# Optimization experiments

Hardware: AMD Instinct MI355X
Metric: run time of the kernel (lower is better)

The kernel has to match this reference:

```python
import jax, jax.numpy as jnp
import numpy as np

N_NODES = 100000
N_EDGES = 1000000
IN_DIM = 64
OUT_DIM = 64
EDGE_DIM = 16
LN_EPS = 1e-5
GINE_EPS = 0.0  # PyG GINEConv default eps


def setup_inputs() -> dict:
    key = jax.random.key(0)
    ks = jax.random.split(key, 10)
    s = lambda d: 1.0 / np.sqrt(d)
    x = jax.random.normal(ks[0], (N_NODES, IN_DIM), dtype=jnp.float32)
    edge_index = jax.random.randint(ks[1], (2, N_EDGES), 0, N_NODES, dtype=jnp.int64)
    edge_attr = jax.random.normal(ks[2], (N_EDGES, EDGE_DIM), dtype=jnp.float32)
    # GINEConv internal edge projection Linear(edge_dim, in_dim)
    We = jax.random.uniform(ks[3], (EDGE_DIM, IN_DIM), jnp.float32, -s(EDGE_DIM), s(EDGE_DIM))
    be = jax.random.uniform(ks[4], (IN_DIM,), jnp.float32, -s(EDGE_DIM), s(EDGE_DIM))
    # MLP: Linear(in_dim, out_dim) -> ReLU -> Linear(out_dim, out_dim)
    W1 = jax.random.uniform(ks[5], (IN_DIM, OUT_DIM), jnp.float32, -s(IN_DIM), s(IN_DIM))
    b1 = jax.random.uniform(ks[6], (OUT_DIM,), jnp.float32, -s(IN_DIM), s(IN_DIM))
    W2 = jax.random.uniform(ks[7], (OUT_DIM, OUT_DIM), jnp.float32, -s(OUT_DIM), s(OUT_DIM))
    b2 = jax.random.uniform(ks[8], (OUT_DIM,), jnp.float32, -s(OUT_DIM), s(OUT_DIM))
    ln_gamma = jnp.ones((OUT_DIM,), jnp.float32)
    ln_beta = jnp.zeros((OUT_DIM,), jnp.float32)
    return {"x": x, "edge_index": edge_index, "edge_attr": edge_attr,
            "We": We, "be": be, "W1": W1, "b1": b1, "W2": W2, "b2": b2,
            "ln_gamma": ln_gamma, "ln_beta": ln_beta}


def reference(x, edge_index, edge_attr, We, be, W1, b1, W2, b2, ln_gamma, ln_beta):
    src, dst = edge_index[0], edge_index[1]
    # message: ReLU(x_j + lin(edge_attr))  [E, IN_DIM]
    msg = jax.nn.relu(x[src] + edge_attr @ We + be)
    # scatter-sum into target nodes  [N, IN_DIM]
    aggr = jax.ops.segment_sum(msg, dst, num_segments=x.shape[0])
    h = (1.0 + GINE_EPS) * x + aggr
    # MLP
    h = jax.nn.relu(h @ W1 + b1) @ W2 + b2
    # LayerNorm over last dim
    mu = jnp.mean(h, axis=-1, keepdims=True)
    var = jnp.var(h, axis=-1, keepdims=True)
    h = (h - mu) * jax.lax.rsqrt(var + LN_EPS) * ln_gamma + ln_beta
    return jax.nn.relu(h)
```

## Files before the change

kernel.cpp:

```cpp
#include <hip/hip_runtime.h>

typedef short short8 __attribute__((ext_vector_type(8)));
typedef float f32x4 __attribute__((ext_vector_type(4)));

__device__ __forceinline__ float bf2f(unsigned short b) {
    union { unsigned u; float f; } c;
    c.u = ((unsigned)b) << 16;
    return c.f;
}

__device__ __forceinline__ unsigned short f2bf(float x) {
    union { float f; unsigned u; } c;
    c.f = x;
    unsigned u = c.u;
    u += 0x7fffu + ((u >> 16) & 1u);
    return (unsigned short)(u >> 16);
}

__device__ __forceinline__ float loadf(const void* p, long long i, unsigned isbf) {
    if (isbf) return bf2f(((const unsigned short*)p)[i]);
    return ((const float*)p)[i];
}

__device__ __forceinline__ f32x4 mfma16(short8 a, short8 b, f32x4 c) {
    return __builtin_amdgcn_mfma_f32_16x16x32_bf16(a, b, c, 0, 0, 0);
}

__device__ __forceinline__ float dotbf(uint4 ea, uint4 eb, const float* Wcol) {
    unsigned wds[8] = {ea.x, ea.y, ea.z, ea.w, eb.x, eb.y, eb.z, eb.w};
    float acc = 0.f;
    #pragma unroll
    for (int q = 0; q < 8; ++q) {
        union { unsigned u; float f; } clo, chi;
        clo.u = wds[q] << 16;
        chi.u = wds[q] & 0xffff0000u;
        acc += clo.f * Wcol[2 * q] + chi.f * Wcol[2 * q + 1];
    }
    return acc;
}

__device__ __forceinline__ float dotf32(const float* eap, const float* Wcol) {
    f32x4 e0 = ((const f32x4*)eap)[0];
    f32x4 e1 = ((const f32x4*)eap)[1];
    f32x4 e2 = ((const f32x4*)eap)[2];
    f32x4 e3 = ((const f32x4*)eap)[3];
    float ea[16] = {e0[0], e0[1], e0[2], e0[3],
                    e1[0], e1[1], e1[2], e1[3],
                    e2[0], e2[1], e2[2], e2[3],
                    e3[0], e3[1], e3[2], e3[3]};
    float acc = 0.f;
    #pragma unroll
    for (int k = 0; k < 16; ++k) acc += ea[k] * Wcol[k];
    return acc;
}

__global__ void gine_flag_kernel(const unsigned* gm_bits, const unsigned* ei_bits,
                                 unsigned* flags) {
    if (blockIdx.x == 0 && threadIdx.x == 0) {
        flags[0] = (gm_bits[0] == 0x3F803F80u) ? 1u : 0u;
        unsigned o = 0;
        for (int k = 0; k < 8; ++k) o |= ei_bits[2 * k + 1];
        flags[1] = (o == 0u) ? 1u : 0u;
    }
}

__global__ void gine_zero_kernel(float* p, int n) {
    int t = blockIdx.x * blockDim.x + threadIdx.x;
    if (t < n) p[t] = 0.0f;
}

__global__ void gine_prep_kernel(const void* W1, const void* b1,
                                 const void* W2, const void* b2,
                                 const void* gm, const void* bt,
                                 const void* We, const void* be,
                                 const unsigned* flags,
                                 unsigned short* W1B, unsigned short* W2B,
                                 float* vecs) {
    int t = blockIdx.x * blockDim.x + threadIdx.x;
    unsigned isbf = flags[0];
    if (t < 8192) {
        int which = t >> 12;
        int u = t & 4095;
        int j = u & 7, L = (u >> 3) & 63, ktnt = u >> 9;
        int kt = ktnt >> 2, nt = ktnt & 3;
        int k = kt * 32 + (L >> 4) * 8 + j;
        int c = nt * 16 + (L & 15);
        const void* W = which ? W2 : W1;
        unsigned short v = f2bf(loadf(W, k * 64 + c, isbf));
        if (which) W2B[u] = v; else W1B[u] = v;
    } else if (t < 8448) {
        int u = t - 8192;
        const void* s = (u < 64) ? b1 : (u < 128) ? b2 : (u < 192) ? gm : bt;
        vecs[u] = loadf(s, u & 63, isbf);
    } else if (t < 8512) {
        vecs[256 + (t - 8448)] = loadf(be, t - 8448, isbf);
    } else if (t < 9536) {
        int u = t - 8512;
        vecs[320 + u] = loadf(We, u, isbf);
    }
}

__global__ void gine_hist_kernel(const void* edge_index, const unsigned* flags,
                                 int* count, int E, int N) {
    int t = blockIdx.x * blockDim.x + threadIdx.x;
    int stride = gridDim.x * blockDim.x;
    unsigned is64 = flags[1];
    for (int e = t; e < E; e += stride) {
        long long dst = is64 ? ((const long long*)edge_index)[E + e]
                             : (long long)((const int*)edge_index)[E + e];
        if (dst >= 0 && dst < N) atomicAdd(&count[(int)dst], 1);
    }
}

__global__ void gine_scan1_kernel(const int* count, int* row_start, int* bsum,
                                  int N) {
    __shared__ int s[256];
    int t = threadIdx.x;
    int i = blockIdx.x * 256 + t;
    int v = (i < N) ? count[i] : 0;
    s[t] = v;
    __syncthreads();
    for (int off = 1; off < 256; off <<= 1) {
        int u = (t >= off) ? s[t - off] : 0;
        __syncthreads();
        s[t] += u;
        __syncthreads();
    }
    if (i < N) row_start[i] = s[t] - v;
    if (t == 255) bsum[blockIdx.x] = s[255];
}

__global__ void gine_scan2_kernel(int* bsum, int* bscan, int* row_start,
                                  int nb, int N) {
    __shared__ int s[512];
    int t = threadIdx.x;
    int v = (t < nb) ? bsum[t] : 0;
    s[t] = v;
    __syncthreads();
    for (int off = 1; off < 512; off <<= 1) {
        int u = (t >= off) ? s[t - off] : 0;
        __syncthreads();
        s[t] += u;
        __syncthreads();
    }
    if (t < nb) bscan[t] = s[t] - v;
    if (t == nb - 1) row_start[N] = s[t];
}

__global__ void gine_scan3_kernel(int* row_start, int* cursor,
                                  const int* bscan, int N) {
    int i = blockIdx.x * 256 + threadIdx.x;
    if (i < N) {
        int r = row_start[i] + bscan[blockIdx.x];
        row_start[i] = r;
        cursor[i] = r;
    }
}

__global__ void gine_scatter_kernel(const void* edge_index, const unsigned* flags,
                                    int* cursor, unsigned long long* sorted,
                                    int E, int N) {
    int t = blockIdx.x * blockDim.x + threadIdx.x;
    int stride = gridDim.x * blockDim.x;
    unsigned is64 = flags[1];
    for (int e = t; e < E; e += stride) {
        long long src, dst;
        if (is64) {
            src = ((const long long*)edge_index)[e];
            dst = ((const long long*)edge_index)[E + e];
        } else {
            src = ((const int*)edge_index)[e];
            dst = ((const int*)edge_index)[E + e];
        }
        if (dst < 0 || dst >= N) continue;
        if (src < 0) src = 0;
        if (src >= N) src = N - 1;
        int pos = atomicAdd(&cursor[(int)dst], 1);
        sorted[pos] = ((unsigned long long)(unsigned)e << 32) | (unsigned long long)(unsigned)src;
    }
}

__global__ __launch_bounds__(256, 4) void gine_gather_kernel(
        const void* x, const void* edge_attr,
        const unsigned long long* sorted,
        const int* row_start, const float* vecs,
        const unsigned* flags, float* h, int N) {
    int w = threadIdx.x >> 6;
    int lane = threadIdx.x & 63;
    int gw = blockIdx.x * 4 + w;
    int nwaves = gridDim.x * 4;
    unsigned isbf = flags[0];

    float Wcol[16];
    #pragma unroll
    for (int k = 0; k < 16; ++k) Wcol[k] = vecs[320 + k * 64 + lane];
    float bev = vecs[256 + lane];

    if (isbf) {
        const unsigned short* xb  = (const unsigned short*)x;
        const unsigned short* eab = (const unsigned short*)edge_attr;
        for (int v = gw; v < N; v += nwaves) {
            int beg = row_start[v];
            int end = row_start[v + 1];
            float a0 = bf2f(xb[(size_t)v * 64 + lane]);
            float a1 = 0.f, a2 = 0.f, a3 = 0.f;
            int i = beg;
            for (; i + 4 <= end; i += 4) {
                unsigned long long c0 = sorted[i];
                unsigned long long c1 = sorted[i + 1];
                unsigned long long c2 = sorted[i + 2];
                unsigned long long c3 = sorted[i + 3];
                int src0 = (int)(c0 & 0xffffffffULL), eid0 = (int)(c0 >> 32);
                int src1 = (int)(c1 & 0xffffffffULL), eid1 = (int)(c1 >> 32);
                int src2 = (int)(c2 & 0xffffffffULL), eid2 = (int)(c2 >> 32);
                int src3 = (int)(c3 & 0xffffffffULL), eid3 = (int)(c3 >> 32);

                float xv0 = bf2f(xb[(size_t)src0 * 64 + lane]);
                float xv1 = bf2f(xb[(size_t)src1 * 64 + lane]);
                float xv2 = bf2f(xb[(size_t)src2 * 64 + lane]);
                float xv3 = bf2f(xb[(size_t)src3 * 64 + lane]);

                const uint4* p0 = (const uint4*)(eab + (size_t)eid0 * 16);
                const uint4* p1 = (const uint4*)(eab + (size_t)eid1 * 16);
                const uint4* p2 = (const uint4*)(eab + (size_t)eid2 * 16);
                const uint4* p3 = (const uint4*)(eab + (size_t)eid3 * 16);
                uint4 e00 = p0[0], e01 = p0[1];
                uint4 e10 = p1[0], e11 = p1[1];
                uint4 e20 = p2[0], e21 = p2[1];
                uint4 e30 = p3[0], e31 = p3[1];

                float m0 = dotbf(e00, e01, Wcol);
                float m1 = dotbf(e10, e11, Wcol);
                float m2 = dotbf(e20, e21, Wcol);
                float m3 = dotbf(e30, e31, Wcol);
                m0 += bev + xv0; if (m0 < 0.f) m0 = 0.f; a0 += m0;
                m1 += bev + xv1; if (m1 < 0.f) m1 = 0.f; a1 += m1;
                m2 += bev + xv2; if (m2 < 0.f) m2 = 0.f; a2 += m2;
                m3 += bev + xv3; if (m3 < 0.f) m3 = 0.f; a3 += m3;
            }
            for (; i < end; ++i) {
                unsigned long long c = sorted[i];
                int src = (int)(c & 0xffffffffULL);
                int eid = (int)(c >> 32);
                float xv = bf2f(xb[(size_t)src * 64 + lane]);
                const uint4* p0 = (const uint4*)(eab + (size_t)eid * 16);
                uint4 e0 = p0[0], e1 = p0[1];
                float m = dotbf(e0, e1, Wcol);
                m += bev + xv;
                if (m < 0.f) m = 0.f;
                a0 += m;
            }
            h[(long long)v * 64 + lane] = (a0 + a1) + (a2 + a3);
        }
    } else {
        const float* xf  = (const float*)x;
        const float* eaf = (const float*)edge_attr;
        for (int v = gw; v < N; v += nwaves) {
            int beg = row_start[v];
            int end = row_start[v + 1];
            float a0 = xf[(size_t)v * 64 + lane];
            float a1 = 0.f;
            int i = beg;
            for (; i + 2 <= end; i += 2) {
                unsigned long long c0 = sorted[i];
                unsigned long long c1 = sorted[i + 1];
                int src0 = (int)(c0 & 0xffffffffULL), eid0 = (int)(c0 >> 32);
                int src1 = (int)(c1 & 0xffffffffULL), eid1 = (int)(c1 >> 32);
                float xv0 = xf[(size_t)src0 * 64 + lane];
                float xv1 = xf[(size_t)src1 * 64 + lane];
                float m0 = dotf32(eaf + (size_t)eid0 * 16, Wcol);
                float m1 = dotf32(eaf + (size_t)eid1 * 16, Wcol);
                m0 += bev + xv0; if (m0 < 0.f) m0 = 0.f; a0 += m0;
                m1 += bev + xv1; if (m1 < 0.f) m1 = 0.f; a1 += m1;
            }
            for (; i < end; ++i) {
                unsigned long long c = sorted[i];
                int src = (int)(c & 0xffffffffULL);
                int eid = (int)(c >> 32);
                float xv = xf[(size_t)src * 64 + lane];
                float m = dotf32(eaf + (size_t)eid * 16, Wcol);
                m += bev + xv;
                if (m < 0.f) m = 0.f;
                a0 += m;
            }
            h[(long long)v * 64 + lane] = a0 + a1;
        }
    }
}

__global__ void GINEBlock_49795850830259_kernel(
    const void* x, const void* edge_index, const void* edge_attr,
    const void* We, const void* be, const unsigned* flags,
    float* aggr, int E, int N, int n0, int n1) {
    int wid  = (blockIdx.x * blockDim.x + threadIdx.x) >> 6;
    int lane = threadIdx.x & 63;
    if (wid >= E) return;

    unsigned isbf = flags[0];
    unsigned is64 = flags[1];

    long long src, dst;
    if (is64) {
        src = ((const long long*)edge_index)[wid];
        dst = ((const long long*)edge_index)[E + wid];
    } else {
        src = ((const int*)edge_index)[wid];
        dst = ((const int*)edge_index)[E + wid];
    }
    if (src < 0 || src >= N || dst < n0 || dst >= n1) return;

    float eav = 0.0f;
    if (lane < 16) eav = loadf(edge_attr, (long long)wid * 16 + lane, isbf);

    float acc = loadf(be, lane, isbf);
    for (int k = 0; k < 16; ++k)
        acc += __shfl(eav, k, 64) * loadf(We, k * 64 + lane, isbf);

    acc += loadf(x, src * 64 + lane, isbf);
    if (acc < 0.0f) acc = 0.0f;

    atomicAdd(aggr + (dst - n0) * 64 + lane, acc);
}

__global__ void gine_addx_kernel(const void* x, float* aggr,
                                 const unsigned* flags, int n0, int n1) {
    int t = blockIdx.x * blockDim.x + threadIdx.x;
    int total = (n1 - n0) * 64;
    if (t >= total) return;
    unsigned isbf = flags[0];
    aggr[t] += loadf(x, (long long)n0 * 64 + t, isbf);
}

__global__ __launch_bounds__(256) void gine_node_mfma_kernel(
    const float* h, const unsigned short* W1B, const unsigned short* W2B,
    const float* vecs, const unsigned* flags, void* out, int n0, int n1) {
    __shared__ float Tlds[4][16 * 68];
    int w = threadIdx.x >> 6;
    int L = threadIdx.x & 63;
    int g = L >> 4, m = L & 15;
    int nb = n0 + (blockIdx.x * 4 + w) * 16;
    if (nb >= n1) return;
    unsigned isbf = flags[0];

    const float* b1f = vecs;
    const float* b2f = vecs + 64;
    const float* gmf = vecs + 128;
    const float* btf = vecs + 192;

    int node = nb + m;
    if (node >= n1) node = n1 - 1;
    long long rel = node - n0;

    short8 ahi[2], alo[2];
    for (int kt = 0; kt < 2; ++kt) {
        int fb = kt * 32 + g * 8;
        const float* hp = h + rel * 64 + fb;
        f32x4 a0 = *(const f32x4*)hp;
        f32x4 a1 = *(const f32x4*)(hp + 4);
        for (int j = 0; j < 8; ++j) {
            float hv = (j < 4) ? a0[j] : a1[j - 4];
            unsigned short hb = f2bf(hv);
            float lo = hv - bf2f(hb);
            ahi[kt][j] = (short)hb;
            alo[kt][j] = (short)f2bf(lo);
        }
    }

    float t16[16];
    for (int nt = 0; nt < 4; ++nt) {
        short8 bp0 = *(const short8*)(W1B + ((size_t)(0 * 4 + nt) * 64 + L) * 8);
        short8 bp1 = *(const short8*)(W1B + ((size_t)(1 * 4 + nt) * 64 + L) * 8);
        f32x4 acc = {0.f, 0.f, 0.f, 0.f};
        acc = mfma16(ahi[0], bp0, acc);
        acc = mfma16(ahi[1], bp1, acc);
        acc = mfma16(alo[0], bp0, acc);
        acc = mfma16(alo[1], bp1, acc);
        float bias = b1f[nt * 16 + m];
        for (int r = 0; r < 4; ++r) {
            float v = acc[r] + bias;
            t16[nt * 4 + r] = v > 0.f ? v : 0.f;
        }
    }

    float* tl = Tlds[w];
    for (int nt = 0; nt < 4; ++nt)
        for (int r = 0; r < 4; ++r)
            tl[(g * 4 + r) * 68 + nt * 16 + m] = t16[nt * 4 + r];

    short8 thi[2], tlo[2];
    for (int kt = 0; kt < 2; ++kt) {
        const float* rp = tl + m * 68 + kt * 32 + g * 8;
        f32x4 v0 = *(const f32x4*)rp;
        f32x4 v1 = *(const f32x4*)(rp + 4);
        for (int j = 0; j < 8; ++j) {
            float hv = (j < 4) ? v0[j] : v1[j - 4];
            unsigned short hb = f2bf(hv);
            float lo = hv - bf2f(hb);
            thi[kt][j] = (short)hb;
            tlo[kt][j] = (short)f2bf(lo);
        }
    }

    float o16[16];
    for (int nt = 0; nt < 4; ++nt) {
        short8 bp0 = *(const short8*)(W2B + ((size_t)(0 * 4 + nt) * 64 + L) * 8);
        short8 bp1 = *(const short8*)(W2B + ((size_t)(1 * 4 + nt) * 64 + L) * 8);
        f32x4 acc = {0.f, 0.f, 0.f, 0.f};
        acc = mfma16(thi[0], bp0, acc);
        acc = mfma16(thi[1], bp1, acc);
        acc = mfma16(tlo[0], bp0, acc);
        acc = mfma16(tlo[1], bp1, acc);
        float bias = b2f[nt * 16 + m];
        for (int r = 0; r < 4; ++r) o16[nt * 4 + r] = acc[r] + bias;
    }

    for (int r = 0; r < 4; ++r) {
        float s = o16[r] + o16[4 + r] + o16[8 + r] + o16[12 + r];
        s += __shfl_xor(s, 1, 64);
        s += __shfl_xor(s, 2, 64);
        s += __shfl_xor(s, 4, 64);
        s += __shfl_xor(s, 8, 64);
        float mu = s * (1.0f / 64.0f);
        float v = 0.f;
        for (int nt = 0; nt < 4; ++nt) {
            float d = o16[nt * 4 + r] - mu;
            v += d * d;
        }
        v += __shfl_xor(v, 1, 64);
        v += __shfl_xor(v, 2, 64);
        v += __shfl_xor(v, 4, 64);
        v += __shfl_xor(v, 8, 64);
        float inv = rsqrtf(v * (1.0f / 64.0f) + 1e-5f);
        int nodeR = nb + g * 4 + r;
        if (nodeR < n1) {
            for (int nt = 0; nt < 4; ++nt) {
                int c = nt * 16 + m;
                float rr = (o16[nt * 4 + r] - mu) * inv * gmf[c] + btf[c];
                if (rr < 0.f) rr = 0.f;
                long long oidx = (long long)nodeR * 64 + c;
                if (isbf) ((unsigned short*)out)[oidx] = f2bf(rr);
                else      ((float*)out)[oidx] = rr;
            }
        }
    }
}

static inline size_t align256(size_t a) { return (a + 255) & ~(size_t)255; }

extern "C" void kernel_launch(void* const* d_in, const int* in_sizes, int n_in,
                              void* d_out, int out_size, void* d_ws, size_t ws_size,
                              hipStream_t stream) {
    const void* x          = d_in[0];
    const void* edge_index = d_in[1];
    const void* edge_attr  = d_in[2];
    const void* We         = d_in[3];
    const void* be         = d_in[4];
    const void* W1         = d_in[5];
    const void* b1         = d_in[6];
    const void* W2         = d_in[7];
    const void* b2         = d_in[8];
    const void* gm         = d_in[9];
    const void* bt         = d_in[10];

    const int N = in_sizes[0] / 64;
    const int E = in_sizes[1] / 2;

    unsigned* flags     = (unsigned*)d_ws;
    unsigned short* W1B = (unsigned short*)((char*)d_ws + 256);
    unsigned short* W2B = W1B + 4096;
    float* vecs         = (float*)(W2B + 4096);
    int* bsum           = (int*)((char*)d_ws + 24576);
    int* bscan          = bsum + 1024;

    gine_flag_kernel<<<1, 64, 0, stream>>>((const unsigned*)gm,
                                           (const unsigned*)edge_index, flags);
    gine_prep_kernel<<<38, 256, 0, stream>>>(W1, b1, W2, b2, gm, bt, We, be,
                                             flags, W1B, W2B, vecs);

    int nb = (N + 255) / 256;
    int node_blocks = (N + 63) / 64;
    int gblocks = (N + 15) / 16;
    if (gblocks > 6250) gblocks = 6250;

    size_t o_count  = 32768;
    size_t o_row    = o_count + align256((size_t)N * 4);
    size_t o_cursor = o_row + align256((size_t)(N + 1) * 4);
    size_t o_sorted = o_cursor + align256((size_t)N * 4);
    size_t o_h      = o_sorted + align256((size_t)E * 8);
    size_t need     = o_h + (size_t)N * 256;

    if (ws_size >= need && nb <= 512) {
        int* count    = (int*)((char*)d_ws + o_count);
        int* row_start= (int*)((char*)d_ws + o_row);
        int* cursor   = (int*)((char*)d_ws + o_cursor);
        unsigned long long* sorted = (unsigned long long*)((char*)d_ws + o_sorted);
        float* h      = (float*)((char*)d_ws + o_h);

        gine_zero_kernel<<<(N + 255) / 256, 256, 0, stream>>>((float*)count, N);
        gine_hist_kernel<<<1024, 256, 0, stream>>>(edge_index, flags, count, E, N);
        gine_scan1_kernel<<<nb, 256, 0, stream>>>(count, row_start, bsum, N);
        gine_scan2_kernel<<<1, 512, 0, stream>>>(bsum, bscan, row_start, nb, N);
        gine_scan3_kernel<<<nb, 256, 0, stream>>>(row_start, cursor, bscan, N);
        gine_scatter_kernel<<<1024, 256, 0, stream>>>(edge_index, flags, cursor,
                                                      sorted, E, N);
        gine_gather_kernel<<<gblocks, 256, 0, stream>>>(x, edge_attr, sorted,
                                                        row_start, vecs, flags, h, N);
        gine_node_mfma_kernel<<<node_blocks, 256, 0, stream>>>(
            h, W1B, W2B, vecs, flags, d_out, 0, N);
        return;
    }

    float* aggr = (float*)((char*)d_ws + 32768);
    long long usable = (ws_size > 32768) ? (long long)(ws_size - 32768) : 0;
    long long ncll = (usable / 256) & ~63LL;
    int NC = (ncll > N) ? N : (int)ncll;
    if (NC < 64) return;

    long long edge_threads = (long long)E * 64;
    int edge_blocks = (int)((edge_threads + 255) / 256);

    for (int n0 = 0; n0 < N; n0 += NC) {
        int n1 = n0 + NC; if (n1 > N) n1 = N;
        int chunk = n1 - n0;
        int n_aggr = chunk * 64;

        gine_zero_kernel<<<(n_aggr + 255) / 256, 256, 0, stream>>>(aggr, n_aggr);
        GINEBlock_49795850830259_kernel<<<edge_blocks, 256, 0, stream>>>(
            x, edge_index, edge_attr, We, be, flags, aggr, E, N, n0, n1);
        gine_addx_kernel<<<(n_aggr + 255) / 256, 256, 0, stream>>>(
            x, aggr, flags, n0, n1);
        int chunk_blocks = (chunk + 63) / 64;
        gine_node_mfma_kernel<<<chunk_blocks, 256, 0, stream>>>(
            aggr, W1B, W2B, vecs, flags, d_out, n0, n1);
    }
}
```

Measured before the change: 465.9 us.

## Permute edge attributes into destination-sorted order during scatter for contiguous gather reads

The scatter kernel now also copies each edge's bf16 attribute row into a buffer indexed by its sorted position, so the gather kernel reads edge attributes contiguously instead of through random edge ids. This converts the random edge_attr reads in the gather into streaming reads, at the cost of an extra 32 MB write and read plus a random-destination write during the scatter. The gather unroll drops from 4 to 2 and the occupancy hint is removed. The new path runs only when the workspace is large enough and the input is bf16.

Result: no change. 460.6 us, median of 2 (-1.1%).

```diff
diff --git a/kernel.cpp b/kernel.cpp
--- a/kernel.cpp
+++ b/kernel.cpp
@@ -180,9 +180,43 @@
     }
 }
 
-__global__ __launch_bounds__(256, 4) void gine_gather_kernel(
+__global__ void gine_scatter2_kernel(const void* edge_index, const void* edge_attr,
+                                     const unsigned* flags,
+                                     int* cursor, unsigned long long* sorted,
+                                     unsigned short* ea_perm, int E, int N) {
+    int t = blockIdx.x * blockDim.x + threadIdx.x;
+    int stride = gridDim.x * blockDim.x;
+    unsigned is64 = flags[1];
+    unsigned isbf = flags[0];
+    for (int e = t; e < E; e += stride) {
+        long long src, dst;
+        if (is64) {
+            src = ((const long long*)edge_index)[e];
+            dst = ((const long long*)edge_index)[E + e];
+        } else {
+            src = ((const int*)edge_index)[e];
+            dst = ((const int*)edge_index)[E + e];
+        }
+        if (dst < 0 || dst >= N) continue;
+        if (src < 0) src = 0;
+        if (src >= N) src = N - 1;
+        int pos = atomicAdd(&cursor[(int)dst], 1);
+        sorted[pos] = ((unsigned long long)(unsigned)e << 32) | (unsigned long long)(unsigned)src;
+        if (isbf) {
+            const uint4* er = (const uint4*)((const unsigned short*)edge_attr
+                                             + (size_t)e * 16);
+            uint4 r0 = er[0];
+            uint4 r1 = er[1];
+            uint4* wp = (uint4*)(ea_perm + (size_t)pos * 16);
+            wp[0] = r0;
+            wp[1] = r1;
+        }
+    }
+}
+
+__global__ __launch_bounds__(256) void gine_gather2_kernel(
         const void* x, const void* edge_attr,
-        const unsigned long long* sorted,
+        const unsigned long long* sorted, const unsigned short* ea_perm,
         const int* row_start, const float* vecs,
         const unsigned* flags, float* h, int N) {
     int w = threadIdx.x >> 6;
@@ -197,60 +231,43 @@
     float bev = vecs[256 + lane];
 
     if (isbf) {
-        const unsigned short* xb  = (const unsigned short*)x;
-        const unsigned short* eab = (const unsigned short*)edge_attr;
+        const unsigned short* xb = (const unsigned short*)x;
         for (int v = gw; v < N; v += nwaves) {
             int beg = row_start[v];
             int end = row_start[v + 1];
             float a0 = bf2f(xb[(size_t)v * 64 + lane]);
-            float a1 = 0.f, a2 = 0.f, a3 = 0.f;
+            float a1 = 0.f;
             int i = beg;
-            for (; i + 4 <= end; i += 4) {
+            for (; i + 2 <= end; i += 2) {
                 unsigned long long c0 = sorted[i];
                 unsigned long long c1 = sorted[i + 1];
-                unsigned long long c2 = sorted[i + 2];
-                unsigned long long c3 = sorted[i + 3];
-                int src0 = (int)(c0 & 0xffffffffULL), eid0 = (int)(c0 >> 32);
-                int src1 = (int)(c1 & 0xffffffffULL), eid1 = (int)(c1 >> 32);
-                int src2 = (int)(c2 & 0xffffffffULL), eid2 = (int)(c2 >> 32);
-                int src3 = (int)(c3 & 0xffffffffULL), eid3 = (int)(c3 >> 32);
+                int src0 = (int)(c0 & 0xffffffffULL);
+                int src1 = (int)(c1 & 0xffffffffULL);
+
+                const uint4* p = (const uint4*)(ea_perm + (size_t)i * 16);
+                uint4 e00 = p[0], e01 = p[1];
+                uint4 e10 = p[2], e11 = p[3];
 
                 float xv0 = bf2f(xb[(size_t)src0 * 64 + lane]);
                 float xv1 = bf2f(xb[(size_t)src1 * 64 + lane]);
-                float xv2 = bf2f(xb[(size_t)src2 * 64 + lane]);
-                float xv3 = bf2f(xb[(size_t)src3 * 64 + lane]);
-
-                const uint4* p0 = (const uint4*)(eab + (size_t)eid0 * 16);
-                const uint4* p1 = (const uint4*)(eab + (size_t)eid1 * 16);
-                const uint4* p2 = (const uint4*)(eab + (size_t)eid2 * 16);
-                const uint4* p3 = (const uint4*)(eab + (size_t)eid3 * 16);
-                uint4 e00 = p0[0], e01 = p0[1];
-                uint4 e10 = p1[0], e11 = p1[1];
-                uint4 e20 = p2[0], e21 = p2[1];
-                uint4 e30 = p3[0], e31 = p3[1];
 
                 float m0 = dotbf(e00, e01, Wcol);
                 float m1 = dotbf(e10, e11, Wcol);
-                float m2 = dotbf(e20, e21, Wcol);
-                float m3 = dotbf(e30, e31, Wcol);
                 m0 += bev + xv0; if (m0 < 0.f) m0 = 0.f; a0 += m0;
                 m1 += bev + xv1; if (m1 < 0.f) m1 = 0.f; a1 += m1;
-                m2 += bev + xv2; if (m2 < 0.f) m2 = 0.f; a2 += m2;
-                m3 += bev + xv3; if (m3 < 0.f) m3 = 0.f; a3 += m3;
             }
             for (; i < end; ++i) {
                 unsigned long long c = sorted[i];
                 int src = (int)(c & 0xffffffffULL);
-                int eid = (int)(c >> 32);
+                const uint4* p = (const uint4*)(ea_perm + (size_t)i * 16);
+                uint4 e0 = p[0], e1 = p[1];
                 float xv = bf2f(xb[(size_t)src * 64 + lane]);
-                const uint4* p0 = (const uint4*)(eab + (size_t)eid * 16);
-                uint4 e0 = p0[0], e1 = p0[1];
                 float m = dotbf(e0, e1, Wcol);
                 m += bev + xv;
                 if (m < 0.f) m = 0.f;
                 a0 += m;
             }
-            h[(long long)v * 64 + lane] = (a0 + a1) + (a2 + a3);
+            h[(long long)v * 64 + lane] = a0 + a1;
         }
     } else {
         const float* xf  = (const float*)x;
@@ -288,6 +305,114 @@
     }
 }
 
+__global__ __launch_bounds__(256, 4) void gine_gather_kernel(
+        const void* x, const void* edge_attr,
+        const unsigned long long* sorted,
+        const int* row_start, const float* vecs,
+        const unsigned* flags, float* h, int N) {
+    int w = threadIdx.x >> 6;
+    int lane = threadIdx.x & 63;
+    int gw = blockIdx.x * 4 + w;
+    int nwaves = gridDim.x * 4;
+    unsigned isbf = flags[0];
+
+    float Wcol[16];
+    #pragma unroll
+    for (int k = 0; k < 16; ++k) Wcol[k] = vecs[320 + k * 64 + lane];
+    float bev = vecs[256 + lane];
+
+    if (isbf) {
+        const unsigned short* xb  = (const unsigned short*)x;
+        const unsigned short* eab = (const unsigned short*)edge_attr;
+        for (int v = gw; v < N; v += nwaves) {
+            int beg = row_start[v];
+            int end = row_start[v + 1];
+            float a0 = bf2f(xb[(size_t)v * 64 + lane]);
+            float a1 = 0.f, a2 = 0.f, a3 = 0.f;
+            int i = beg;
+            for (; i + 4 <= end; i += 4) {
+                unsigned long long c0 = sorted[i];
+                unsigned long long c1 = sorted[i + 1];
+                unsigned long long c2 = sorted[i + 2];
+                unsigned long long c3 = sorted[i + 3];
+                int src0 = (int)(c0 & 0xffffffffULL), eid0 = (int)(c0 >> 32);
+                int src1 = (int)(c1 & 0xffffffffULL), eid1 = (int)(c1 >> 32);
+                int src2 = (int)(c2 & 0xffffffffULL), eid2 = (int)(c2 >> 32);
+                int src3 = (int)(c3 & 0xffffffffULL), eid3 = (int)(c3 >> 32);
+
+                float xv0 = bf2f(xb[(size_t)src0 * 64 + lane]);
+                float xv1 = bf2f(xb[(size_t)src1 * 64 + lane]);
+                float xv2 = bf2f(xb[(size_t)src2 * 64 + lane]);
+                float xv3 = bf2f(xb[(size_t)src3 * 64 + lane]);
+
+                const uint4* p0 = (const uint4*)(eab + (size_t)eid0 * 16);
+                const uint4* p1 = (const uint4*)(eab + (size_t)eid1 * 16);
+                const uint4* p2 = (const uint4*)(eab + (size_t)eid2 * 16);
+                const uint4* p3 = (const uint4*)(eab + (size_t)eid3 * 16);
+                uint4 e00 = p0[0], e01 = p0[1];
+                uint4 e10 = p1[0], e11 = p1[1];
+                uint4 e20 = p2[0], e21 = p2[1];
+                uint4 e30 = p3[0], e31 = p3[1];
+
+                float m0 = dotbf(e00, e01, Wcol);
+                float m1 = dotbf(e10, e11, Wcol);
+                float m2 = dotbf(e20, e21, Wcol);
+                float m3 = dotbf(e30, e31, Wcol);
+                m0 += bev + xv0; if (m0 < 0.f) m0 = 0.f; a0 += m0;
+                m1 += bev + xv1; if (m1 < 0.f) m1 = 0.f; a1 += m1;
+                m2 += bev + xv2; if (m2 < 0.f) m2 = 0.f; a2 += m2;
+                m3 += bev + xv3; if (m3 < 0.f) m3 = 0.f; a3 += m3;
+            }
+            for (; i < end; ++i) {
+                unsigned long long c = sorted[i];
+                int src = (int)(c & 0xffffffffULL);
+                int eid = (int)(c >> 32);
+                float xv = bf2f(xb[(size_t)src * 64 + lane]);
+                const uint4* p0 = (const uint4*)(eab + (size_t)eid * 16);
+                uint4 e0 = p0[0], e1 = p0[1];
+                float m = dotbf(e0, e1, Wcol);
+                m += bev + xv;
+                if (m < 0.f) m = 0.f;
+                a0 += m;
+            }
+            h[(long long)v * 64 + lane] = (a0 + a1) + (a2 + a3);
+        }
+    } else {
+        const float* xf  = (const float*)x;
+        const float* eaf = (const float*)edge_attr;
+        for (int v = gw; v < N; v += nwaves) {
+            int beg = row_start[v];
+            int end = row_start[v + 1];
+            float a0 = xf[(size_t)v * 64 + lane];
+            float a1 = 0.f;
+            int i = beg;
+            for (; i + 2 <= end; i += 2) {
+                unsigned long long c0 = sorted[i];
+                unsigned long long c1 = sorted[i + 1];
+                int src0 = (int)(c0 & 0xffffffffULL), eid0 = (int)(c0 >> 32);
+                int src1 = (int)(c1 & 0xffffffffULL), eid1 = (int)(c1 >> 32);
+                float xv0 = xf[(size_t)src0 * 64 + lane];
+                float xv1 = xf[(size_t)src1 * 64 + lane];
+                float m0 = dotf32(eaf + (size_t)eid0 * 16, Wcol);
+                float m1 = dotf32(eaf + (size_t)eid1 * 16, Wcol);
+                m0 += bev + xv0; if (m0 < 0.f) m0 = 0.f; a0 += m0;
+                m1 += bev + xv1; if (m1 < 0.f) m1 = 0.f; a1 += m1;
+            }
+            for (; i < end; ++i) {
+                unsigned long long c = sorted[i];
+                int src = (int)(c & 0xffffffffULL);
+                int eid = (int)(c >> 32);
+                float xv = xf[(size_t)src * 64 + lane];
+                float m = dotf32(eaf + (size_t)eid * 16, Wcol);
+                m += bev + xv;
+                if (m < 0.f) m = 0.f;
+                a0 += m;
+            }
+            h[(long long)v * 64 + lane] = a0 + a1;
+        }
+    }
+}
+
 __global__ void GINEBlock_49795850830259_kernel(
     const void* x, const void* edge_index, const void* edge_attr,
     const void* We, const void* be, const unsigned* flags,
@@ -486,25 +611,40 @@
     size_t o_row    = o_count + align256((size_t)N * 4);
     size_t o_cursor = o_row + align256((size_t)(N + 1) * 4);
     size_t o_sorted = o_cursor + align256((size_t)N * 4);
-    size_t o_h      = o_sorted + align256((size_t)E * 8);
-    size_t need     = o_h + (size_t)N * 256;
-
-    if (ws_size >= need && nb <= 512) {
+    size_t o_eap    = o_sorted + align256((size_t)E * 8);
+    size_t o_h1     = o_eap;
+    size_t o_h2     = o_eap + align256((size_t)E * 32);
+    size_t need1    = o_h1 + (size_t)N * 256;
+    size_t need2    = o_h2 + (size_t)N * 256;
+
+    if (ws_size >= need1 && nb <= 512) {
         int* count    = (int*)((char*)d_ws + o_count);
         int* row_start= (int*)((char*)d_ws + o_row);
         int* cursor   = (int*)((char*)d_ws + o_cursor);
         unsigned long long* sorted = (unsigned long long*)((char*)d_ws + o_sorted);
-        float* h      = (float*)((char*)d_ws + o_h);
+        bool tier2 = (ws_size >= need2);
+        unsigned short* ea_perm = (unsigned short*)((char*)d_ws + o_eap);
+        float* h = (float*)((char*)d_ws + (tier2 ? o_h2 : o_h1));
 
         gine_zero_kernel<<<(N + 255) / 256, 256, 0, stream>>>((float*)count, N);
         gine_hist_kernel<<<1024, 256, 0, stream>>>(edge_index, flags, count, E, N);
         gine_scan1_kernel<<<nb, 256, 0, stream>>>(count, row_start, bsum, N);
         gine_scan2_kernel<<<1, 512, 0, stream>>>(bsum, bscan, row_start, nb, N);
         gine_scan3_kernel<<<nb, 256, 0, stream>>>(row_start, cursor, bscan, N);
-        gine_scatter_kernel<<<1024, 256, 0, stream>>>(edge_index, flags, cursor,
-                                                      sorted, E, N);
-        gine_gather_kernel<<<gblocks, 256, 0, stream>>>(x, edge_attr, sorted,
-                                                        row_start, vecs, flags, h, N);
+        if (tier2) {
+            gine_scatter2_kernel<<<1024, 256, 0, stream>>>(edge_index, edge_attr,
+                                                           flags, cursor, sorted,
+                                                           ea_perm, E, N);
+            gine_gather2_kernel<<<gblocks, 256, 0, stream>>>(x, edge_attr, sorted,
+                                                             ea_perm, row_start,
+                                                             vecs, flags, h, N);
+        } else {
+            gine_scatter_kernel<<<1024, 256, 0, stream>>>(edge_index, flags, cursor,
+                                                          sorted, E, N);
+            gine_gather_kernel<<<gblocks, 256, 0, stream>>>(x, edge_attr, sorted,
+                                                            row_start, vecs, flags,
+                                                            h, N);
+        }
         gine_node_mfma_kernel<<<node_blocks, 256, 0, stream>>>(
             h, W1B, W2B, vecs, flags, d_out, 0, N);
         return;
```

## Sort edges by source and scatter messages via atomics instead of dst-gather

Applied to the files above, without the earlier changes.

Replaces the destination-sorted gather with a source-sorted 'spray': edges are bucketed by source node, each wave loads the source node's x row once and atomically adds ReLU messages into h rows of destination nodes, with h pre-initialised from x. The scatter step also copies edge_attr rows into source-sorted order, bf16 only, so the spray reads them contiguously. This trades per-edge random x reads for per-edge random fp32 atomic adds and an extra edge_attr copy, and the atomics make the summation order nondeterministic. The old path is kept as a fallback when the workspace is too small.

New measurement: 530.9 us, median of 2. 14.0% more time.

```diff
diff --git a/kernel.cpp b/kernel.cpp
--- a/kernel.cpp
+++ b/kernel.cpp
@@ -100,15 +100,49 @@
     }
 }
 
-__global__ void gine_hist_kernel(const void* edge_index, const unsigned* flags,
-                                 int* count, int E, int N) {
+__global__ void gine_hinit_kernel(const void* x, float* h,
+                                  const unsigned* flags, int total) {
+    int t = blockIdx.x * blockDim.x + threadIdx.x;
+    unsigned isbf = flags[0];
+    if (isbf) {
+        int i = t * 8;
+        if (i >= total) return;
+        uint4 v = *(const uint4*)((const unsigned short*)x + i);
+        unsigned wds[4] = {v.x, v.y, v.z, v.w};
+        #pragma unroll
+        for (int q = 0; q < 4; ++q) {
+            union { unsigned u; float f; } clo, chi;
+            clo.u = wds[q] << 16;
+            chi.u = wds[q] & 0xffff0000u;
+            h[i + 2 * q]     = clo.f;
+            h[i + 2 * q + 1] = chi.f;
+        }
+    } else {
+        int i = t * 4;
+        if (i >= total) return;
+        f32x4 v = *(const f32x4*)((const float*)x + i);
+        *(f32x4*)(h + i) = v;
+    }
+}
+
+__global__ void gine_histS_kernel(const void* edge_index, const unsigned* flags,
+                                  int* count, int E, int N) {
     int t = blockIdx.x * blockDim.x + threadIdx.x;
     int stride = gridDim.x * blockDim.x;
     unsigned is64 = flags[1];
     for (int e = t; e < E; e += stride) {
-        long long dst = is64 ? ((const long long*)edge_index)[E + e]
-                             : (long long)((const int*)edge_index)[E + e];
-        if (dst >= 0 && dst < N) atomicAdd(&count[(int)dst], 1);
+        long long src, dst;
+        if (is64) {
+            src = ((const long long*)edge_index)[e];
+            dst = ((const long long*)edge_index)[E + e];
+        } else {
+            src = ((const int*)edge_index)[e];
+            dst = ((const int*)edge_index)[E + e];
+        }
+        if (dst < 0 || dst >= N) continue;
+        if (src < 0) src = 0;
+        if (src >= N) src = N - 1;
+        atomicAdd(&count[(int)src], 1);
     }
 }
 
@@ -154,6 +188,122 @@
         int r = row_start[i] + bscan[blockIdx.x];
         row_start[i] = r;
         cursor[i] = r;
+    }
+}
+
+__global__ void gine_scatterS_kernel(const void* edge_index, const void* edge_attr,
+                                     const unsigned* flags, int* cursor,
+                                     unsigned long long* meta,
+                                     unsigned short* eaS, int E, int N) {
+    int t = blockIdx.x * blockDim.x + threadIdx.x;
+    int stride = gridDim.x * blockDim.x;
+    unsigned is64 = flags[1];
+    unsigned isbf = flags[0];
+    for (int e = t; e < E; e += stride) {
+        long long src, dst;
+        if (is64) {
+            src = ((const long long*)edge_index)[e];
+            dst = ((const long long*)edge_index)[E + e];
+        } else {
+            src = ((const int*)edge_index)[e];
+            dst = ((const int*)edge_index)[E + e];
+        }
+        if (dst < 0 || dst >= N) continue;
+        if (src < 0) src = 0;
+        if (src >= N) src = N - 1;
+        int pos = atomicAdd(&cursor[(int)src], 1);
+        meta[pos] = ((unsigned long long)(unsigned)e << 32)
+                  | (unsigned long long)(unsigned)dst;
+        if (isbf) {
+            const uint4* er = (const uint4*)((const unsigned short*)edge_attr
+                                             + (size_t)e * 16);
+            uint4 r0 = er[0];
+            uint4 r1 = er[1];
+            uint4* wp = (uint4*)(eaS + (size_t)pos * 16);
+            wp[0] = r0;
+            wp[1] = r1;
+        }
+    }
+}
+
+__global__ __launch_bounds__(256) void gine_spray_kernel(
+        const void* x, const void* edge_attr,
+        const unsigned long long* meta, const unsigned short* eaS,
+        const int* rowS, const float* vecs, const unsigned* flags,
+        float* h, int N) {
+    int w = threadIdx.x >> 6;
+    int lane = threadIdx.x & 63;
+    int gw = blockIdx.x * 4 + w;
+    int nwaves = gridDim.x * 4;
+    unsigned isbf = flags[0];
+
+    float Wcol[16];
+    #pragma unroll
+    for (int k = 0; k < 16; ++k) Wcol[k] = vecs[320 + k * 64 + lane];
+    float bev = vecs[256 + lane];
+
+    if (isbf) {
+        const unsigned short* xb = (const unsigned short*)x;
+        for (int s = gw; s < N; s += nwaves) {
+            int beg = rowS[s];
+            int end = rowS[s + 1];
+            if (beg == end) continue;
+            float xv = bf2f(xb[(size_t)s * 64 + lane]) + bev;
+            int j = beg;
+            for (; j + 2 <= end; j += 2) {
+                unsigned long long m0m = meta[j];
+                unsigned long long m1m = meta[j + 1];
+                int dst0 = (int)(m0m & 0xffffffffULL);
+                int dst1 = (int)(m1m & 0xffffffffULL);
+                const uint4* p = (const uint4*)(eaS + (size_t)j * 16);
+                uint4 e00 = p[0], e01 = p[1];
+                uint4 e10 = p[2], e11 = p[3];
+                float m0 = dotbf(e00, e01, Wcol) + xv;
+                float m1 = dotbf(e10, e11, Wcol) + xv;
+                if (m0 < 0.f) m0 = 0.f;
+                if (m1 < 0.f) m1 = 0.f;
+                atomicAdd(&h[(size_t)dst0 * 64 + lane], m0);
+                atomicAdd(&h[(size_t)dst1 * 64 + lane], m1);
+            }
+            if (j < end) {
+                unsigned long long mm = meta[j];
+                int dst = (int)(mm & 0xffffffffULL);
+                const uint4* p = (const uint4*)(eaS + (size_t)j * 16);
+                uint4 e0 = p[0], e1 = p[1];
+                float m = dotbf(e0, e1, Wcol) + xv;
+                if (m < 0.f) m = 0.f;
+                atomicAdd(&h[(size_t)dst * 64 + lane], m);
+            }
+        }
+    } else {
+        const float* xf  = (const float*)x;
+        const float* eaf = (const float*)edge_attr;
+        for (int s = gw; s < N; s += nwaves) {
+            int beg = rowS[s];
+            int end = rowS[s + 1];
+            if (beg == end) continue;
+            float xv = xf[(size_t)s * 64 + lane] + bev;
+            for (int j = beg; j < end; ++j) {
+                unsigned long long mm = meta[j];
+                int dst = (int)(mm & 0xffffffffULL);
+                int eid = (int)(mm >> 32);
+                float m = dotf32(eaf + (size_t)eid * 16, Wcol) + xv;
+                if (m < 0.f) m = 0.f;
+                atomicAdd(&h[(size_t)dst * 64 + lane], m);
+            }
+        }
+    }
+}
+
+__global__ void gine_hist_kernel(const void* edge_index, const unsigned* flags,
+                                 int* count, int E, int N) {
+    int t = blockIdx.x * blockDim.x + threadIdx.x;
+    int stride = gridDim.x * blockDim.x;
+    unsigned is64 = flags[1];
+    for (int e = t; e < E; e += stride) {
+        long long dst = is64 ? ((const long long*)edge_index)[E + e]
+                             : (long long)((const int*)edge_index)[E + e];
+        if (dst >= 0 && dst < N) atomicAdd(&count[(int)dst], 1);
     }
 }
 
@@ -481,20 +631,49 @@
     int node_blocks = (N + 63) / 64;
     int gblocks = (N + 15) / 16;
     if (gblocks > 6250) gblocks = 6250;
+    int total = N * 64;
 
     size_t o_count  = 32768;
     size_t o_row    = o_count + align256((size_t)N * 4);
     size_t o_cursor = o_row + align256((size_t)(N + 1) * 4);
-    size_t o_sorted = o_cursor + align256((size_t)N * 4);
-    size_t o_h      = o_sorted + align256((size_t)E * 8);
-    size_t need     = o_h + (size_t)N * 256;
-
-    if (ws_size >= need && nb <= 512) {
+    size_t o_meta   = o_cursor + align256((size_t)N * 4);
+    size_t o_eas    = o_meta + align256((size_t)E * 8);
+    size_t o_hA     = o_eas + align256((size_t)E * 32);
+    size_t o_hB     = o_eas;
+    size_t needA    = o_hA + (size_t)N * 256;
+    size_t needB    = o_hB + (size_t)N * 256;
+
+    if (ws_size >= needA && nb <= 512) {
+        int* count     = (int*)((char*)d_ws + o_count);
+        int* rowS      = (int*)((char*)d_ws + o_row);
+        int* cursorS   = (int*)((char*)d_ws + o_cursor);
+        unsigned long long* meta = (unsigned long long*)((char*)d_ws + o_meta);
+        unsigned short* eaS      = (unsigned short*)((char*)d_ws + o_eas);
+        float* h       = (float*)((char*)d_ws + o_hA);
+
+        gine_zero_kernel<<<(N + 255) / 256, 256, 0, stream>>>((float*)count, N);
+        gine_hinit_kernel<<<(total / 4 + 255) / 256, 256, 0, stream>>>(
+            x, h, flags, total);
+        gine_histS_kernel<<<1024, 256, 0, stream>>>(edge_index, flags, count, E, N);
+        gine_scan1_kernel<<<nb, 256, 0, stream>>>(count, rowS, bsum, N);
+        gine_scan2_kernel<<<1, 512, 0, stream>>>(bsum, bscan, rowS, nb, N);
+        gine_scan3_kernel<<<nb, 256, 0, stream>>>(rowS, cursorS, bscan, N);
+        gine_scatterS_kernel<<<1024, 256, 0, stream>>>(edge_index, edge_attr,
+                                                       flags, cursorS, meta,
+                                                       eaS, E, N);
+        gine_spray_kernel<<<gblocks, 256, 0, stream>>>(x, edge_attr, meta, eaS,
+                                                       rowS, vecs, flags, h, N);
+        gine_node_mfma_kernel<<<node_blocks, 256, 0, stream>>>(
+            h, W1B, W2B, vecs, flags, d_out, 0, N);
+        return;
+    }
+
+    if (ws_size >= needB && nb <= 512) {
         int* count    = (int*)((char*)d_ws + o_count);
         int* row_start= (int*)((char*)d_ws + o_row);
         int* cursor   = (int*)((char*)d_ws + o_cursor);
-        unsigned long long* sorted = (unsigned long long*)((char*)d_ws + o_sorted);
-        float* h      = (float*)((char*)d_ws + o_h);
+        unsigned long long* sorted = (unsigned long long*)((char*)d_ws + o_meta);
+        float* h      = (float*)((char*)d_ws + o_hB);
 
         gine_zero_kernel<<<(N + 255) / 256, 256, 0, stream>>>((float*)count, N);
         gine_hist_kernel<<<1024, 256, 0, stream>>>(edge_index, flags, count, E, N);
@@ -504,7 +683,8 @@
         gine_scatter_kernel<<<1024, 256, 0, stream>>>(edge_index, flags, cursor,
                                                       sorted, E, N);
         gine_gather_kernel<<<gblocks, 256, 0, stream>>>(x, edge_attr, sorted,
-                                                        row_start, vecs, flags, h, N);
+                                                        row_start, vecs, flags,
+                                                        h, N);
         gine_node_mfma_kernel<<<node_blocks, 256, 0, stream>>>(
             h, W1B, W2B, vecs, flags, d_out, 0, N);
         return;
```
